# Performance work log

Measured on AMD Instinct MI355X. Metric: run time of the kernel, lower is better.

## Reference

```python
import jax, jax.numpy as jnp
import numpy as np

HID = 128
NUM_HEADS = 8
NUM_LAYERS = 3
N_OP, N_MA, N_JOB = 50000, 1000, 5000
E_SIZES = [150000, 100000, 150000, 100000, 100000]
# (src_type, dst_type) for the 5 edge relations, in module order:
# precedence, assigned_to, can_process, contains, belongs_to
EDGE_SD = [("operation", "operation"), ("operation", "machine"), ("machine", "operation"), ("job", "operation"), ("operation", "job")]
NT_IDX = {"operation": 0, "machine": 1, "job": 2}


def setup_inputs() -> dict:
    key = jax.random.key(0)
    ks = list(jax.random.split(key, 80))
    it = iter(ks)

    def nrm(shape, scale=1.0):
        return jax.random.normal(next(it), shape, dtype=jnp.float32) * scale

    n_nodes = {"operation": N_OP, "machine": N_MA, "job": N_JOB}
    inp = {}
    inp["x_operation"] = nrm((N_OP, 64))
    inp["x_machine"] = nrm((N_MA, 32))
    inp["x_job"] = nrm((N_JOB, 16))
    ei_names = ["ei_prec", "ei_assign", "ei_canproc", "ei_contains", "ei_belongs"]
    ea_names = ["ea_prec", "ea_assign", "ea_canproc", "ea_contains", "ea_belongs"]
    for ne, na, E, (st, dt) in zip(ei_names, ea_names, E_SIZES, EDGE_SD):
        src = jax.random.randint(next(it), (E,), 0, n_nodes[st], dtype=jnp.int32)
        dst = jax.random.randint(next(it), (E,), 0, n_nodes[dt], dtype=jnp.int32)
        inp[ne] = jnp.stack([src, dst])
        inp[na] = nrm((E, 32))
    # node input projections (per-type dims)
    inp["Wn_op"] = nrm((64, HID), 64 ** -0.5)
    inp["bn_op"] = jnp.zeros((HID,), jnp.float32)
    inp["Wn_ma"] = nrm((32, HID), 32 ** -0.5)
    inp["bn_ma"] = jnp.zeros((HID,), jnp.float32)
    inp["Wn_job"] = nrm((16, HID), 16 ** -0.5)
    inp["bn_job"] = jnp.zeros((HID,), jnp.float32)
    # edge attr projections: 5 relations, 32 -> HID, applied once before the layers
    inp["We_proj"] = nrm((5, 32, HID), 32 ** -0.5)
    inp["be_proj"] = jnp.zeros((5, HID), jnp.float32)
    # GATConv params stacked as [layer, edge_type, ...]; heads*out == HID at every layer
    inp["Wg"] = nrm((NUM_LAYERS, 5, HID, HID), HID ** -0.5)      # shared lin for src/dst
    inp["att_s"] = nrm((NUM_LAYERS, 5, HID), HID ** -0.5)
    inp["att_d"] = nrm((NUM_LAYERS, 5, HID), HID ** -0.5)
    inp["Wge"] = nrm((NUM_LAYERS, 5, HID, HID), HID ** -0.5)     # lin_edge
    inp["att_e"] = nrm((NUM_LAYERS, 5, HID), HID ** -0.5)
    inp["bg"] = jnp.zeros((NUM_LAYERS, 5, HID), jnp.float32)      # GATConv output bias
    # BatchNorm affine: [layer, node_type, HID]
    inp["gamma"] = jnp.ones((NUM_LAYERS, 3, HID), jnp.float32)
    inp["beta"] = jnp.zeros((NUM_LAYERS, 3, HID), jnp.float32)
    # output projection for 'operation'
    inp["Wo"] = nrm((HID, HID), HID ** -0.5)
    inp["bo"] = jnp.zeros((HID,), jnp.float32)
    return inp


def _segment_softmax(logits, seg, num):
    # PyG softmax: exp(x - segment_max) / (segment_sum + 1e-16)
    m = jax.ops.segment_max(logits, seg, num_segments=num)
    m = jnp.where(jnp.isfinite(m), m, 0.0)  # empty segments -> 0
    ex = jnp.exp(logits - m[seg])
    den = jax.ops.segment_sum(ex, seg, num_segments=num)
    return ex / (den[seg] + 1e-16)


def _gat_forward(x_operation, x_machine, x_job, eis, eas_raw,
                 Wn_op, bn_op, Wn_ma, bn_ma, Wn_job, bn_job,
                 We_proj, be_proj, Wg, att_s, att_d, Wge, att_e, bg,
                 gamma, beta, Wo, bo):
    x = {
        "operation": x_operation @ Wn_op + bn_op,
        "machine": x_machine @ Wn_ma + bn_ma,
        "job": x_job @ Wn_job + bn_job,
    }
    # edge attrs projected once to HID
    eas = [eas_raw[t] @ We_proj[t] + be_proj[t] for t in range(5)]

    for i in range(NUM_LAYERS):
        H = NUM_HEADS if i < NUM_LAYERS - 1 else 1
        C = HID // H
        resid = x
        agg = {nt: jnp.zeros((x[nt].shape[0], HID), x[nt].dtype) for nt in x}
        for t, (st, dt) in enumerate(EDGE_SD):
            src, dst = eis[t][0], eis[t][1]
            n_dst = x[dt].shape[0]
            xs = (x[st] @ Wg[i, t]).reshape(-1, H, C)            # [Ns,H,C]
            xd = (x[dt] @ Wg[i, t]).reshape(-1, H, C)            # [Nd,H,C]
            a_s = (xs * att_s[i, t].reshape(H, C)).sum(-1)       # [Ns,H]
            a_d = (xd * att_d[i, t].reshape(H, C)).sum(-1)       # [Nd,H]
            e = (eas[t] @ Wge[i, t]).reshape(-1, H, C)           # [E,H,C]
            a_e = (e * att_e[i, t].reshape(H, C)).sum(-1)        # [E,H]
            logits = jax.nn.leaky_relu(a_s[src] + a_d[dst] + a_e, 0.2)
            alpha = _segment_softmax(logits, dst, n_dst)         # [E,H]
            msg = xs[src] * alpha[:, :, None]                    # [E,H,C]
            out = jax.ops.segment_sum(msg, dst, num_segments=n_dst)
            agg[dt] = agg[dt] + out.reshape(n_dst, HID) + bg[i, t]
        new_x = {}
        for nt in x:
            h = agg[nt]
            mu = h.mean(0)
            var = ((h - mu) ** 2).mean(0)  # biased, as BatchNorm1d training
            h = (h - mu) * jax.lax.rsqrt(var + 1e-5) * gamma[i, NT_IDX[nt]] + beta[i, NT_IDX[nt]]
            if i < NUM_LAYERS - 1:
                h = jax.nn.relu(h)  # dropout is identity in eval
            new_x[nt] = h + resid[nt]  # residual (dims always match: HID)
        x = new_x
    return x["operation"] @ Wo + bo


def reference(x_operation, x_machine, x_job,
              ei_prec, ei_assign, ei_canproc, ei_contains, ei_belongs,
              ea_prec, ea_assign, ea_canproc, ea_contains, ea_belongs,
              Wn_op, bn_op, Wn_ma, bn_ma, Wn_job, bn_job,
              We_proj, be_proj, Wg, att_s, att_d, Wge, att_e, bg,
              gamma, beta, Wo, bo):
    eis = [ei_prec, ei_assign, ei_canproc, ei_contains, ei_belongs]
    eas = [ea_prec, ea_assign, ea_canproc, ea_contains, ea_belongs]
    return _gat_forward(x_operation, x_machine, x_job, eis, eas,
                        Wn_op, bn_op, Wn_ma, bn_ma, Wn_job, bn_job,
                        We_proj, be_proj, Wg, att_s, att_d, Wge, att_e, bg,
                        gamma, beta, Wo, bo)
```

## Files before the change

kernel.cpp:

```cpp
#include <hip/hip_runtime.h>
#include <cstdint>

#define HID 128

static constexpr int kNOp = 50000, kNMa = 1000, kNJob = 5000;
static constexpr int kNTot = 56000;
static constexpr int kETot = 600000;
static constexpr int kSeg = 156000;
static constexpr int kEsz[5]   = {150000, 100000, 150000, 100000, 100000};
static constexpr int kSrcT[5]  = {0, 0, 1, 2, 0};
static constexpr int kDstT[5]  = {0, 1, 0, 0, 2};
static constexpr int kNodeOff[3] = {0, 50000, 51000};
static constexpr int kSoff[5]  = {0, 0, 50000, 51000, 0};
static constexpr int kDoff[5]  = {0, 50000, 0, 0, 51000};
static constexpr int kEoff[6]  = {0, 150000, 250000, 400000, 500000, 600000};
static constexpr int kRoff[5]  = {0, 50000, 100000, 101000, 106000};
static constexpr int kRTot = 156000;

typedef __attribute__((ext_vector_type(8))) __bf16 bf16x8;
typedef __attribute__((ext_vector_type(4))) float f32x4;

__device__ inline unsigned short f2b(float f) {
  unsigned u = __float_as_uint(f);
  unsigned r = (u + 0x7FFFu + ((u >> 16) & 1u)) >> 16;
  return (unsigned short)r;
}
__device__ inline float b2f(unsigned short u) {
  return __uint_as_float(((unsigned)u) << 16);
}

__device__ inline int seg_of(int t, int d) {
  if (t == 0) return 3 * d;
  if (t == 2) return 3 * d + 1;
  if (t == 3) return 3 * d + 2;
  if (t == 1) return 150000 + d;
  return 151000 + d;
}

__global__ void conv_pad(const float* __restrict__ in, unsigned short* __restrict__ out,
                         int M, int K, int Kp) {
  int i = blockIdx.x * blockDim.x + threadIdx.x;
  if (i >= M * Kp) return;
  int r = i / Kp, c = i - r * Kp;
  out[i] = (c < K) ? f2b(in[(size_t)r * K + c]) : (unsigned short)0;
}

__global__ void transpose_w(const float* __restrict__ W, unsigned short* __restrict__ Wt,
                            int K, int N, int Kp, int nmat) {
  int i = blockIdx.x * blockDim.x + threadIdx.x;
  int per = N * Kp;
  if (i >= nmat * per) return;
  int b = i / per, rem = i - b * per;
  int n = rem / Kp, k = rem - n * Kp;
  Wt[i] = (k < K) ? f2b(W[(size_t)b * K * N + (size_t)k * N + n]) : (unsigned short)0;
}

template <int KC>
__global__ __launch_bounds__(256) void gemm_mfma(
    const unsigned short* __restrict__ A, const unsigned short* __restrict__ Bt,
    const float* __restrict__ bias, float* __restrict__ Cf,
    unsigned short* __restrict__ Cb, int M) {
  const int K = KC * 32;
  int w = blockIdx.x * 4 + (threadIdx.x >> 6);
  int m0 = w * 16;
  if (m0 >= M) return;
  int lane = threadIdx.x & 63;
  int l16 = lane & 15, quad = lane >> 4;
  int arow = m0 + l16; if (arow >= M) arow = M - 1;
  bf16x8 af[KC];
#pragma unroll
  for (int kc = 0; kc < KC; kc++) {
    int4 raw = *(const int4*)(A + (size_t)arow * K + kc * 32 + quad * 8);
    af[kc] = __builtin_bit_cast(bf16x8, raw);
  }
#pragma unroll
  for (int nt = 0; nt < 8; nt++) {
    int col = nt * 16 + l16;
    f32x4 acc = {0.f, 0.f, 0.f, 0.f};
#pragma unroll
    for (int kc = 0; kc < KC; kc++) {
      int4 braw = *(const int4*)(Bt + (size_t)col * K + kc * 32 + quad * 8);
      acc = __builtin_amdgcn_mfma_f32_16x16x32_bf16(
          af[kc], __builtin_bit_cast(bf16x8, braw), acc, 0, 0, 0);
    }
    float bv = bias ? bias[col] : 0.f;
#pragma unroll
    for (int r = 0; r < 4; r++) {
      int row = m0 + quad * 4 + r;
      if (row < M) {
        float v = acc[r] + bv;
        if (Cf) Cf[(size_t)row * HID + col] = v;
        if (Cb) Cb[(size_t)row * HID + col] = f2b(v);
      }
    }
  }
}

struct GemmJobs {
  const unsigned short* A[5];
  const unsigned short* Bt[5];
  unsigned short* Cb[5];
  int M[5];
  int bpref[6];
};

__global__ __launch_bounds__(256) void gemm_batched(GemmJobs J) {
  int b = blockIdx.x;
  int t = 0;
  while (t < 4 && b >= J.bpref[t + 1]) t++;
  const int M = J.M[t];
  int strip = (b - J.bpref[t]) * 4 + (threadIdx.x >> 6);
  int m0 = strip * 16;
  if (m0 >= M) return;
  int lane = threadIdx.x & 63;
  int l16 = lane & 15, quad = lane >> 4;
  const unsigned short* A = J.A[t];
  const unsigned short* Bt = J.Bt[t];
  unsigned short* Cb = J.Cb[t];
  int arow = m0 + l16; if (arow >= M) arow = M - 1;
  bf16x8 af[4];
#pragma unroll
  for (int kc = 0; kc < 4; kc++) {
    int4 raw = *(const int4*)(A + (size_t)arow * HID + kc * 32 + quad * 8);
    af[kc] = __builtin_bit_cast(bf16x8, raw);
  }
#pragma unroll
  for (int nt = 0; nt < 8; nt++) {
    int col = nt * 16 + l16;
    f32x4 acc = {0.f, 0.f, 0.f, 0.f};
#pragma unroll
    for (int kc = 0; kc < 4; kc++) {
      int4 braw = *(const int4*)(Bt + (size_t)col * HID + kc * 32 + quad * 8);
      acc = __builtin_amdgcn_mfma_f32_16x16x32_bf16(
          af[kc], __builtin_bit_cast(bf16x8, braw), acc, 0, 0, 0);
    }
#pragma unroll
    for (int r = 0; r < 4; r++) {
      int row = m0 + quad * 4 + r;
      if (row < M) Cb[(size_t)row * HID + col] = f2b(acc[r]);
    }
  }
}

template <int NCOL>
__global__ __launch_bounds__(256) void gemm_as(
    const unsigned short* __restrict__ A, const unsigned short* __restrict__ Bt,
    float* __restrict__ out, int M) {
  int w = blockIdx.x * 4 + (threadIdx.x >> 6);
  int m0 = w * 16;
  if (m0 >= M) return;
  int lane = threadIdx.x & 63;
  int l16 = lane & 15, quad = lane >> 4;
  int arow = m0 + l16; if (arow >= M) arow = M - 1;
  bf16x8 af[4];
#pragma unroll
  for (int kc = 0; kc < 4; kc++) {
    int4 raw = *(const int4*)(A + (size_t)arow * HID + kc * 32 + quad * 8);
    af[kc] = __builtin_bit_cast(bf16x8, raw);
  }
#pragma unroll
  for (int nt = 0; nt < NCOL / 16; nt++) {
    int col = nt * 16 + l16;
    f32x4 acc = {0.f, 0.f, 0.f, 0.f};
#pragma unroll
    for (int kc = 0; kc < 4; kc++) {
      int4 braw = *(const int4*)(Bt + (size_t)col * HID + kc * 32 + quad * 8);
      acc = __builtin_amdgcn_mfma_f32_16x16x32_bf16(
          af[kc], __builtin_bit_cast(bf16x8, braw), acc, 0, 0, 0);
    }
#pragma unroll
    for (int r = 0; r < 4; r++) {
      int row = m0 + quad * 4 + r;
      if (row < M) out[(size_t)row * NCOL + col] = acc[r];
    }
  }
}

__global__ void fold_kernel(const float* __restrict__ Wg, const float* __restrict__ att_s,
                            const float* __restrict__ att_d, const float* __restrict__ Wge,
                            const float* __restrict__ att_e, const float* __restrict__ Wep,
                            const float* __restrict__ bep,
                            float* __restrict__ S, float* __restrict__ D,
                            float* __restrict__ w32, float* __restrict__ cvec) {
  int idx = blockIdx.x;
  int h = idx & 7, lt = idx >> 3;
  int l = lt / 5;
  int H = (l < 2) ? 8 : 1, C = HID / H;
  if (h >= H) return;
  int k = threadIdx.x;
  int t = lt % 5;
  const float* wg  = Wg  + (size_t)lt * HID * HID;
  const float* wge = Wge + (size_t)lt * HID * HID;
  const float* as_ = att_s + (size_t)lt * HID + h * C;
  const float* ad_ = att_d + (size_t)lt * HID + h * C;
  const float* ae_ = att_e + (size_t)lt * HID + h * C;
  float s = 0.f, d = 0.f, v = 0.f;
  for (int c = 0; c < C; c++) {
    float wr = wg[(size_t)k * HID + h * C + c];
    s += wr * as_[c];
    d += wr * ad_[c];
    v += wge[(size_t)k * HID + h * C + c] * ae_[c];
  }
  S[(size_t)idx * HID + k] = s;
  D[(size_t)idx * HID + k] = d;
  __shared__ float vs[HID];
  vs[k] = v;
  __syncthreads();
  if (k < 32) {
    const float* wp = Wep + (size_t)t * 32 * HID + (size_t)k * HID;
    float a = 0.f;
    for (int j = 0; j < HID; j++) a += wp[j] * vs[j];
    w32[(size_t)idx * 32 + k] = a;
  }
  if (k == 32) {
    const float* bp = bep + (size_t)t * HID;
    float a = 0.f;
    for (int j = 0; j < HID; j++) a += bp[j] * vs[j];
    cvec[idx] = a;
  }
}

__global__ void build_vb(const float* __restrict__ Sv, const float* __restrict__ Dv,
                         unsigned short* __restrict__ VbT) {
  int i = blockIdx.x * 256 + threadIdx.x;
  if (i >= 3 * 80 * HID) return;
  int l = i / (80 * HID), rem = i % (80 * HID);
  int col = rem / HID, k = rem % HID;
  int H = (l < 2) ? 8 : 1;
  float val = 0.f;
  if (col < 10 * H) {
    int v = col / H, h = col % H;
    const float* base = (v < 5) ? Sv : Dv;
    int t = (v < 5) ? v : v - 5;
    val = base[((size_t)(l * 5 + t) * 8 + h) * HID + k];
  }
  VbT[i] = f2b(val);
}

struct EdgeJobs {
  const int* src[5]; const int* dst[5];
};

__global__ void hist_b(EdgeJobs J, int* __restrict__ cnt) {
  int e = blockIdx.x * 256 + threadIdx.x;
  if (e >= kETot) return;
  int t = 0;
  while (t < 4 && e >= kEoff[t + 1]) t++;
  int d = J.dst[t][e - kEoff[t]];
  atomicAdd(&cnt[seg_of(t, d)], 1);
}

__global__ void scatter_b(EdgeJobs J, int* __restrict__ cursor,
                          int4* __restrict__ edat) {
  int e = blockIdx.x * 256 + threadIdx.x;
  if (e >= kETot) return;
  int t = 0;
  while (t < 4 && e >= kEoff[t + 1]) t++;
  int el = e - kEoff[t];
  int s = J.src[t][el];
  int d = J.dst[t][el];
  int p = atomicAdd(&cursor[seg_of(t, d)], 1);
  edat[p] = make_int4(e, ((s + kSoff[t]) << 3) | t, ((d + kDoff[t]) << 3) | t,
                      s + kRoff[t]);
}

__global__ void scan_blocks(const int* __restrict__ in, int* __restrict__ out,
                            int* __restrict__ bsums, int n) {
  __shared__ int sh[256];
  int t = threadIdx.x;
  int base = blockIdx.x * 1024 + t * 4;
  int v[4]; int s = 0;
#pragma unroll
  for (int j = 0; j < 4; j++) { v[j] = (base + j < n) ? in[base + j] : 0; s += v[j]; }
  sh[t] = s;
  __syncthreads();
  for (int off = 1; off < 256; off <<= 1) {
    int x = (t >= off) ? sh[t - off] : 0;
    __syncthreads();
    sh[t] += x;
    __syncthreads();
  }
  int run = sh[t] - s;
#pragma unroll
  for (int j = 0; j < 4; j++) { if (base + j < n) out[base + j] = run; run += v[j]; }
  if (t == 255) bsums[blockIdx.x] = sh[255];
}

__global__ void scan_carry(int* bsums, int nb, int* sentinel) {
  if (threadIdx.x == 0 && blockIdx.x == 0) {
    int run = 0;
    for (int b = 0; b < nb; b++) { int x = bsums[b]; bsums[b] = run; run += x; }
    *sentinel = run;
  }
}

__global__ void scan_add(int* __restrict__ out, int* __restrict__ cursor,
                         const int* __restrict__ bsums, int n) {
  int base = blockIdx.x * 1024 + threadIdx.x * 4;
  int c = bsums[blockIdx.x];
#pragma unroll
  for (int j = 0; j < 4; j++) {
    if (base + j < n) {
      int v = out[base + j] + c;
      out[base + j] = v;
      cursor[base + j] = v;
    }
  }
}

struct FoldAeJobs {
  const float* ea[5];
  int E[5]; int bpref[6];
};

__global__ __launch_bounds__(256) void fold_ae(FoldAeJobs J, const float* __restrict__ w32,
                                               const float* __restrict__ cv,
                                               float* __restrict__ aet0, float* __restrict__ aet1,
                                               float* __restrict__ aet2) {
  int b = blockIdx.x;
  int t = 0;
  while (t < 4 && b >= J.bpref[t + 1]) t++;
  __shared__ float w[3][8][32];
  __shared__ float cc[3][8];
  for (int i = threadIdx.x; i < 3 * 8 * 32; i += 256) {
    int l = i >> 8, rem = i & 255;
    w[l][rem >> 5][rem & 31] = w32[(size_t)((l * 5 + t) * 8) * 32 + rem];
  }
  if (threadIdx.x < 24) {
    int l = threadIdx.x >> 3, h = threadIdx.x & 7;
    cc[l][h] = cv[(size_t)(l * 5 + t) * 8 + h];
  }
  __syncthreads();
  int e = (b - J.bpref[t]) * 256 + threadIdx.x;
  if (e >= J.E[t]) return;
  int eg = kEoff[t] + e;
  float x[32];
  const float4* p4 = (const float4*)(J.ea[t] + (size_t)e * 32);
#pragma unroll
  for (int i = 0; i < 8; i++) {
    float4 v = p4[i];
    x[4 * i] = v.x; x[4 * i + 1] = v.y; x[4 * i + 2] = v.z; x[4 * i + 3] = v.w;
  }
  float o[8];
#pragma unroll
  for (int h = 0; h < 8; h++) {
    float a = cc[0][h];
#pragma unroll
    for (int k = 0; k < 32; k++) a += x[k] * w[0][h][k];
    o[h] = a;
  }
  float4* d0 = (float4*)(aet0 + (size_t)eg * 8);
  d0[0] = make_float4(o[0], o[1], o[2], o[3]);
  d0[1] = make_float4(o[4], o[5], o[6], o[7]);
#pragma unroll
  for (int h = 0; h < 8; h++) {
    float a = cc[1][h];
#pragma unroll
    for (int k = 0; k < 32; k++) a += x[k] * w[1][h][k];
    o[h] = a;
  }
  float4* d1 = (float4*)(aet1 + (size_t)eg * 8);
  d1[0] = make_float4(o[0], o[1], o[2], o[3]);
  d1[1] = make_float4(o[4], o[5], o[6], o[7]);
  float a = cc[2][0];
#pragma unroll
  for (int k = 0; k < 32; k++) a += x[k] * w[2][0][k];
  aet2[eg] = a;
}

__global__ __launch_bounds__(256) void pass_a8(const int4* __restrict__ edat,
                                               const float* __restrict__ aet,
                                               const float* __restrict__ AS,
                                               float* __restrict__ logits) {
  int p = blockIdx.x * 256 + threadIdx.x;
  if (p >= kETot) return;
  int4 ed = edat[p];
  int e = ed.x, sv = ed.y, dv = ed.z;
  int t = sv & 7;
  const float4* asp = (const float4*)(AS + (size_t)(sv >> 3) * 80 + t * 8);
  const float4* adp = (const float4*)(AS + (size_t)(dv >> 3) * 80 + (5 + t) * 8);
  const float4* aep = (const float4*)(aet + (size_t)e * 8);
  float4 s0 = asp[0], s1 = asp[1];
  float4 d0 = adp[0], d1 = adp[1];
  float4 e0 = aep[0], e1 = aep[1];
  float v[8] = {s0.x + d0.x + e0.x, s0.y + d0.y + e0.y, s0.z + d0.z + e0.z, s0.w + d0.w + e0.w,
                s1.x + d1.x + e1.x, s1.y + d1.y + e1.y, s1.z + d1.z + e1.z, s1.w + d1.w + e1.w};
#pragma unroll
  for (int j = 0; j < 8; j++) v[j] = v[j] > 0.f ? v[j] : 0.2f * v[j];
  float4* L = (float4*)(logits + (size_t)p * 8);
  L[0] = make_float4(v[0], v[1], v[2], v[3]);
  L[1] = make_float4(v[4], v[5], v[6], v[7]);
}

__global__ __launch_bounds__(256) void pass_a1(const int4* __restrict__ edat,
                                               const float* __restrict__ aet2,
                                               const float* __restrict__ AS,
                                               float* __restrict__ logits) {
  int p = blockIdx.x * 256 + threadIdx.x;
  if (p >= kETot) return;
  int4 ed = edat[p];
  int e = ed.x, sv = ed.y, dv = ed.z;
  int t = sv & 7;
  float v = aet2[e] + AS[(size_t)(sv >> 3) * 16 + t] + AS[(size_t)(dv >> 3) * 16 + 5 + t];
  v = v > 0.f ? v : 0.2f * v;
  logits[p] = v;
}

template <int H>
__global__ void softmax_k(const int* __restrict__ rs, float* __restrict__ lg) {
  int g = (int)((blockIdx.x * (size_t)blockDim.x + threadIdx.x) >> 6);
  int lane = threadIdx.x & 63;
  if (g >= kSeg) return;
  int start = rs[g], end = rs[g + 1];
  int n = (end - start) * H;
  if (n == 0) return;
  float* L = lg + (size_t)start * H;
  float m = -3.0e38f;
  for (int idx = lane; idx < n; idx += 64) m = fmaxf(m, L[idx]);
  if (H == 8) {
    m = fmaxf(m, __shfl_xor(m, 8));
    m = fmaxf(m, __shfl_xor(m, 16));
    m = fmaxf(m, __shfl_xor(m, 32));
  } else {
#pragma unroll
    for (int off = 1; off < 64; off <<= 1) m = fmaxf(m, __shfl_xor(m, off));
  }
  float s = 0.f;
  for (int idx = lane; idx < n; idx += 64) {
    float ex = __expf(L[idx] - m);
    L[idx] = ex;
    s += ex;
  }
  if (H == 8) {
    s += __shfl_xor(s, 8);
    s += __shfl_xor(s, 16);
    s += __shfl_xor(s, 32);
  } else {
#pragma unroll
    for (int off = 1; off < 64; off <<= 1) s += __shfl_xor(s, off);
  }
  float inv = 1.f / (s + 1e-16f);
  for (int idx = lane; idx < n; idx += 64) L[idx] *= inv;
}

template <int H>
__global__ void gat_gather_u(const int* __restrict__ rs, const int4* __restrict__ edat,
                             const float* __restrict__ alpha,
                             const unsigned short* __restrict__ xs,
                             float* __restrict__ agg) {
  int g = (int)((blockIdx.x * (size_t)blockDim.x + threadIdx.x) >> 6);
  int lane = threadIdx.x & 63;
  if (g >= kNTot) return;
  int start, end;
  if (g < 50000)      { start = rs[3 * g];              end = rs[3 * g + 3]; }
  else if (g < 51000) { int m = g - 50000; start = rs[150000 + m]; end = rs[150001 + m]; }
  else                { int j = g - 51000; start = rs[151000 + j]; end = rs[151001 + j]; }
  int deg = end - start;
  int l16 = lane & 15, quad = lane >> 4;
  int h = (H == 8) ? (l16 >> 1) : 0;
  float acc[8] = {0.f, 0.f, 0.f, 0.f, 0.f, 0.f, 0.f, 0.f};
  for (int base = 0; base < deg; base += 64) {
    int nchunk = deg - base; if (nchunk > 64) nchunk = 64;
    int sv = (lane < nchunk) ? edat[start + base + lane].w : 0;
    for (int i = 0; i < nchunk; i += 4) {
      int e = i + quad;
      bool act = e < nchunk;
      int s = __shfl(sv, act ? e : 0);
      float w = act ? alpha[(size_t)(start + base + e) * H + h] : 0.f;
      int4 raw = *(const int4*)(xs + (size_t)s * HID + l16 * 8);
      unsigned ua[4] = {(unsigned)raw.x, (unsigned)raw.y, (unsigned)raw.z, (unsigned)raw.w};
#pragma unroll
      for (int j = 0; j < 4; j++) {
        acc[2 * j]     += w * __uint_as_float(ua[j] << 16);
        acc[2 * j + 1] += w * __uint_as_float(ua[j] & 0xFFFF0000u);
      }
    }
  }
#pragma unroll
  for (int j = 0; j < 8; j++) {
    acc[j] += __shfl_xor(acc[j], 16);
    acc[j] += __shfl_xor(acc[j], 32);
  }
  if (quad == 0) {
    float* p = agg + (size_t)g * HID + l16 * 8;
    *(float4*)p = make_float4(acc[0], acc[1], acc[2], acc[3]);
    *(float4*)(p + 4) = make_float4(acc[4], acc[5], acc[6], acc[7]);
  }
}

__global__ void colstats_b(const float* __restrict__ x, float* __restrict__ stats) {
  static constexpr int bpref[4] = {0, 384, 400, 448};
  static constexpr int rowoff[4] = {0, 50000, 51000, 56000};
  int b = blockIdx.x;
  int t = 0;
  while (t < 2 && b >= bpref[t + 1]) t++;
  int bl = b - bpref[t], nb = bpref[t + 1] - bpref[t];
  int tid = threadIdx.x;
  int col = tid & 127, half = tid >> 7;
  float s = 0.f, q = 0.f;
  for (int r = rowoff[t] + bl * 2 + half; r < rowoff[t + 1]; r += nb * 2) {
    float v = x[(size_t)r * HID + col];
    s += v; q += v * v;
  }
  __shared__ float ls[256], lq[256];
  ls[tid] = s; lq[tid] = q;
  __syncthreads();
  if (tid < 128) {
    s = ls[tid] + ls[tid + 128];
    q = lq[tid] + lq[tid + 128];
    unsafeAtomicAdd(&stats[t * 256 + col], s);
    unsafeAtomicAdd(&stats[t * 256 + 128 + col], q);
  }
}

__global__ void bn_apply_b(float* __restrict__ agg, const float* __restrict__ xold,
                           unsigned short* __restrict__ xnb, const float* __restrict__ stats,
                           const float* __restrict__ gammaL, const float* __restrict__ betaL,
                           int relu) {
  size_t i = blockIdx.x * (size_t)blockDim.x + threadIdx.x;
  if (i >= (size_t)kNTot * 32) return;
  int row = (int)(i >> 5);
  int t = (row < 50000) ? 0 : (row < 51000 ? 1 : 2);
  float invN = (t == 0) ? (1.f / 50000.f) : (t == 1 ? (1.f / 1000.f) : (1.f / 5000.f));
  const float* st = stats + t * 256;
  const float* gm = gammaL + t * HID;
  const float* bt = betaL + t * HID;
  int c4 = ((int)(i & 31)) * 4;
  float4 av = ((const float4*)agg)[i];
  float4 xv = ((const float4*)xold)[i];
  float a[4] = {av.x, av.y, av.z, av.w};
  float xo[4] = {xv.x, xv.y, xv.z, xv.w};
  float o[4];
#pragma unroll
  for (int j = 0; j < 4; j++) {
    int c = c4 + j;
    float mu = st[c] * invN;
    float var = st[128 + c] * invN - mu * mu;
    float g = gm[c] * rsqrtf(var + 1e-5f);
    float v = (a[j] - mu) * g + bt[c];
    if (relu) v = fmaxf(v, 0.f);
    o[j] = v + xo[j];
  }
  ((float4*)agg)[i] = make_float4(o[0], o[1], o[2], o[3]);
  ((ushort4*)xnb)[i] = make_ushort4(f2b(o[0]), f2b(o[1]), f2b(o[2]), f2b(o[3]));
}

extern "C" void kernel_launch(void* const* d_in, const int* in_sizes, int n_in,
                              void* d_out, int out_size, void* d_ws, size_t ws_size,
                              hipStream_t stream) {
  const float* x_in[3] = {(const float*)d_in[0], (const float*)d_in[1], (const float*)d_in[2]};
  const int* ei[5];
  const float* ea[5];
  for (int t = 0; t < 5; t++) {
    ei[t] = (const int*)d_in[3 + 2 * t];
    ea[t] = (const float*)d_in[4 + 2 * t];
  }
  const float* Wn[3]  = {(const float*)d_in[13], (const float*)d_in[15], (const float*)d_in[17]};
  const float* bnb[3] = {(const float*)d_in[14], (const float*)d_in[16], (const float*)d_in[18]};
  const float* Wep   = (const float*)d_in[19];
  const float* bep   = (const float*)d_in[20];
  const float* Wg    = (const float*)d_in[21];
  const float* att_s = (const float*)d_in[22];
  const float* att_d = (const float*)d_in[23];
  const float* Wge   = (const float*)d_in[24];
  const float* att_e = (const float*)d_in[25];
  const float* gamma = (const float*)d_in[27];
  const float* beta  = (const float*)d_in[28];
  const float* Wo    = (const float*)d_in[29];
  const float* bo    = (const float*)d_in[30];

  float* ws = (float*)d_ws;
  size_t off = 0;
  auto alloc = [&](size_t n) { size_t o = off; off += (n + 255) & ~(size_t)255; return o; };
  auto allocb = [&](size_t n) { return alloc((n + 1) / 2); };

  float* bufA = ws + alloc((size_t)kNTot * HID);
  float* bufB = ws + alloc((size_t)kNTot * HID);
  unsigned short* xcurb = (unsigned short*)(ws + allocb((size_t)kNTot * HID));
  unsigned short* xs_all = (unsigned short*)(ws + allocb((size_t)kRTot * HID));
  unsigned short* WgT  = (unsigned short*)(ws + allocb((size_t)15 * HID * HID));
  unsigned short* WoT  = (unsigned short*)(ws + allocb((size_t)HID * HID));
  unsigned short* WnT_op  = (unsigned short*)(ws + allocb((size_t)HID * 64));
  unsigned short* WnT_ma  = (unsigned short*)(ws + allocb((size_t)HID * 32));
  unsigned short* WnT_job = (unsigned short*)(ws + allocb((size_t)HID * 32));
  unsigned short* VbT  = (unsigned short*)(ws + allocb((size_t)3 * 80 * HID));
  float* Sv     = ws + alloc((size_t)15 * 8 * HID);
  float* Dv     = ws + alloc((size_t)15 * 8 * HID);
  float* w32    = ws + alloc((size_t)15 * 8 * 32);
  float* cv     = ws + alloc((size_t)15 * 8);
  float* stats  = ws + alloc((size_t)3 * 256);
  float* ASbuf  = ws + alloc((size_t)kNTot * 80);
  float* logits = ws + alloc((size_t)kETot * 8 + 64);
  int* rs_all   = (int*)(ws + alloc((size_t)kSeg + 8));
  int4* edat    = (int4*)(ws + alloc((size_t)kETot * 4));
  float* aet0   = ws + alloc((size_t)kETot * 8);
  float* aet1   = ws + alloc((size_t)kETot * 8);
  float* aet2   = ws + alloc((size_t)kETot);
  unsigned short* xinb_op  = xs_all;
  unsigned short* xinb_ma  = xs_all + 3200000;
  unsigned short* xinb_job = xs_all + 3232000;
  int* cnt    = (int*)logits;
  int* cursor = (int*)(logits + 156032);
  int* bsums  = (int*)(logits + 312064);
  (void)ws_size; (void)in_sizes; (void)n_in; (void)out_size;

  float* xcur = bufA;
  float* agg  = bufB;

  EdgeJobs EJ;
  for (int t = 0; t < 5; t++) { EJ.src[t] = ei[t]; EJ.dst[t] = ei[t] + kEsz[t]; }
  hipMemsetAsync(cnt, 0, (size_t)kSeg * 4, stream);
  hist_b<<<(kETot + 255) / 256, 256, 0, stream>>>(EJ, cnt);
  int nb = (kSeg + 1023) / 1024;
  scan_blocks<<<nb, 256, 0, stream>>>(cnt, rs_all, bsums, kSeg);
  scan_carry<<<1, 64, 0, stream>>>(bsums, nb, rs_all + kSeg);
  scan_add<<<nb, 256, 0, stream>>>(rs_all, cursor, bsums, kSeg);
  scatter_b<<<(kETot + 255) / 256, 256, 0, stream>>>(EJ, cursor, edat);

  conv_pad<<<(kNOp * 64 + 255) / 256, 256, 0, stream>>>(x_in[0], xinb_op, kNOp, 64, 64);
  conv_pad<<<(kNMa * 32 + 255) / 256, 256, 0, stream>>>(x_in[1], xinb_ma, kNMa, 32, 32);
  conv_pad<<<(kNJob * 32 + 255) / 256, 256, 0, stream>>>(x_in[2], xinb_job, kNJob, 16, 32);
  transpose_w<<<(HID * 64 + 255) / 256, 256, 0, stream>>>(Wn[0], WnT_op, 64, HID, 64, 1);
  transpose_w<<<(HID * 32 + 255) / 256, 256, 0, stream>>>(Wn[1], WnT_ma, 32, HID, 32, 1);
  transpose_w<<<(HID * 32 + 255) / 256, 256, 0, stream>>>(Wn[2], WnT_job, 16, HID, 32, 1);
  transpose_w<<<(15 * HID * HID + 255) / 256, 256, 0, stream>>>(Wg, WgT, HID, HID, HID, 15);
  transpose_w<<<(HID * HID + 255) / 256, 256, 0, stream>>>(Wo, WoT, HID, HID, HID, 1);
  fold_kernel<<<120, 128, 0, stream>>>(Wg, att_s, att_d, Wge, att_e, Wep, bep,
                                       Sv, Dv, w32, cv);
  build_vb<<<(3 * 80 * HID + 255) / 256, 256, 0, stream>>>(Sv, Dv, VbT);

  static constexpr int gemmBpref[6]  = {0, 782, 1564, 1580, 1659, 2441};
  static constexpr int foldBpref[6]  = {0, 587, 978, 1565, 1956, 2347};
  static constexpr int nsRel[5] = {50000, 50000, 1000, 5000, 50000};

  FoldAeJobs FJ;
  for (int t = 0; t < 5; t++) {
    FJ.ea[t] = ea[t];
    FJ.E[t] = kEsz[t];
    FJ.bpref[t] = foldBpref[t];
  }
  FJ.bpref[5] = foldBpref[5];
  fold_ae<<<foldBpref[5], 256, 0, stream>>>(FJ, w32, cv, aet0, aet1, aet2);

  gemm_mfma<2><<<((kNOp + 15) / 16 + 3) / 4, 256, 0, stream>>>(
      xinb_op, WnT_op, bnb[0], xcur, xcurb, kNOp);
  gemm_mfma<1><<<((kNMa + 15) / 16 + 3) / 4, 256, 0, stream>>>(
      xinb_ma, WnT_ma, bnb[1], xcur + (size_t)50000 * HID, xcurb + (size_t)50000 * HID, kNMa);
  gemm_mfma<1><<<((kNJob + 15) / 16 + 3) / 4, 256, 0, stream>>>(
      xinb_job, WnT_job, bnb[2], xcur + (size_t)51000 * HID, xcurb + (size_t)51000 * HID, kNJob);

  for (int l = 0; l < 3; l++) {
    int H = (l < 2) ? 8 : 1;

    GemmJobs GJ;
    for (int t = 0; t < 5; t++) {
      int lt = l * 5 + t;
      GJ.A[t]  = xcurb + (size_t)kNodeOff[kSrcT[t]] * HID;
      GJ.Bt[t] = WgT + (size_t)lt * HID * HID;
      GJ.Cb[t] = xs_all + (size_t)kRoff[t] * HID;
      GJ.M[t] = nsRel[t];
      GJ.bpref[t] = gemmBpref[t];
    }
    GJ.bpref[5] = gemmBpref[5];
    gemm_batched<<<gemmBpref[5], 256, 0, stream>>>(GJ);

    int asBlocks = ((kNTot + 15) / 16 + 3) / 4;
    if (H == 8)
      gemm_as<80><<<asBlocks, 256, 0, stream>>>(xcurb, VbT + (size_t)l * 80 * HID, ASbuf, kNTot);
    else
      gemm_as<16><<<asBlocks, 256, 0, stream>>>(xcurb, VbT + (size_t)l * 80 * HID, ASbuf, kNTot);

    int pblocks = (kETot + 255) / 256;
    if (H == 8) {
      const float* aeL = (l == 0) ? aet0 : aet1;
      pass_a8<<<pblocks, 256, 0, stream>>>(edat, aeL, ASbuf, logits);
    } else {
      pass_a1<<<pblocks, 256, 0, stream>>>(edat, aet2, ASbuf, logits);
    }

    if (H == 8) {
      softmax_k<8><<<((size_t)kSeg * 64 + 255) / 256, 256, 0, stream>>>(rs_all, logits);
      gat_gather_u<8><<<((size_t)kNTot * 64 + 255) / 256, 256, 0, stream>>>(
          rs_all, edat, logits, xs_all, agg);
    } else {
      softmax_k<1><<<((size_t)kSeg * 64 + 255) / 256, 256, 0, stream>>>(rs_all, logits);
      gat_gather_u<1><<<((size_t)kNTot * 64 + 255) / 256, 256, 0, stream>>>(
          rs_all, edat, logits, xs_all, agg);
    }

    hipMemsetAsync(stats, 0, 3 * 256 * 4, stream);
    colstats_b<<<448, 256, 0, stream>>>(agg, stats);
    bn_apply_b<<<(unsigned)(((size_t)kNTot * 32 + 255) / 256), 256, 0, stream>>>(
        agg, xcur, xcurb, stats, gamma + (size_t)l * 3 * HID, beta + (size_t)l * 3 * HID,
        (l < 2) ? 1 : 0);
    float* tmp = xcur; xcur = agg; agg = tmp;
  }

  gemm_mfma<4><<<((kNOp + 15) / 16 + 3) / 4, 256, 0, stream>>>(
      xcurb, WoT, bo, (float*)d_out, nullptr, kNOp);
}
```

Baseline: 999.5 us.

## Share operation-row A loads across three relations and vectorize GEMM stores

Replaces the 5-job batched GEMM with a kernel that loads each operation row strip once and computes the three relations whose source is operations (precedence, assigned_to, belongs_to) from the same registers. This cuts the launched blocks from 2441 to 877 and removes redundant A reads. It also swaps the MFMA operand order so each lane holds 4 consecutive output columns of one row, turning scalar stores into vector float4/ushort4 stores in all GEMM kernels. Fewer blocks with three times the work per op-block could lower parallelism and load balance.

```diff
diff --git a/kernel.cpp b/kernel.cpp
--- a/kernel.cpp
+++ b/kernel.cpp
@@ -66,80 +66,80 @@
   if (m0 >= M) return;
   int lane = threadIdx.x & 63;
   int l16 = lane & 15, quad = lane >> 4;
-  int arow = m0 + l16; if (arow >= M) arow = M - 1;
-  bf16x8 af[KC];
+  int xrow = m0 + l16; if (xrow >= M) xrow = M - 1;
+  bf16x8 xf[KC];
 #pragma unroll
   for (int kc = 0; kc < KC; kc++) {
-    int4 raw = *(const int4*)(A + (size_t)arow * K + kc * 32 + quad * 8);
-    af[kc] = __builtin_bit_cast(bf16x8, raw);
-  }
+    int4 raw = *(const int4*)(A + (size_t)xrow * K + kc * 32 + quad * 8);
+    xf[kc] = __builtin_bit_cast(bf16x8, raw);
+  }
+  bool wr = (m0 + l16 < M);
+  int row = m0 + l16;
 #pragma unroll
   for (int nt = 0; nt < 8; nt++) {
-    int col = nt * 16 + l16;
     f32x4 acc = {0.f, 0.f, 0.f, 0.f};
 #pragma unroll
     for (int kc = 0; kc < KC; kc++) {
-      int4 braw = *(const int4*)(Bt + (size_t)col * K + kc * 32 + quad * 8);
+      int4 braw = *(const int4*)(Bt + (size_t)(nt * 16 + l16) * K + kc * 32 + quad * 8);
       acc = __builtin_amdgcn_mfma_f32_16x16x32_bf16(
-          af[kc], __builtin_bit_cast(bf16x8, braw), acc, 0, 0, 0);
-    }
-    float bv = bias ? bias[col] : 0.f;
-#pragma unroll
-    for (int r = 0; r < 4; r++) {
-      int row = m0 + quad * 4 + r;
-      if (row < M) {
-        float v = acc[r] + bv;
-        if (Cf) Cf[(size_t)row * HID + col] = v;
-        if (Cb) Cb[(size_t)row * HID + col] = f2b(v);
-      }
-    }
-  }
-}
-
-struct GemmJobs {
-  const unsigned short* A[5];
-  const unsigned short* Bt[5];
-  unsigned short* Cb[5];
-  int M[5];
-  int bpref[6];
-};
-
-__global__ __launch_bounds__(256) void gemm_batched(GemmJobs J) {
+          __builtin_bit_cast(bf16x8, braw), xf[kc], acc, 0, 0, 0);
+    }
+    int col0 = nt * 16 + quad * 4;
+    float o[4];
+#pragma unroll
+    for (int r = 0; r < 4; r++) o[r] = acc[r] + (bias ? bias[col0 + r] : 0.f);
+    if (wr) {
+      if (Cf) *(float4*)(Cf + (size_t)row * HID + col0) = make_float4(o[0], o[1], o[2], o[3]);
+      if (Cb) *(ushort4*)(Cb + (size_t)row * HID + col0) =
+                  make_ushort4(f2b(o[0]), f2b(o[1]), f2b(o[2]), f2b(o[3]));
+    }
+  }
+}
+
+__global__ __launch_bounds__(256) void gemm_xs(const unsigned short* __restrict__ x,
+                                               const unsigned short* __restrict__ WgTl,
+                                               unsigned short* __restrict__ xs) {
   int b = blockIdx.x;
-  int t = 0;
-  while (t < 4 && b >= J.bpref[t + 1]) t++;
-  const int M = J.M[t];
-  int strip = (b - J.bpref[t]) * 4 + (threadIdx.x >> 6);
+  int grp = (b < 782) ? 0 : (b < 798 ? 1 : 2);
+  int sb   = (grp == 0) ? 0     : (grp == 1 ? 782   : 798);
+  int M    = (grp == 0) ? 50000 : (grp == 1 ? 1000  : 5000);
+  int xoff = (grp == 0) ? 0     : (grp == 1 ? 50000 : 51000);
+  int strip = (b - sb) * 4 + (threadIdx.x >> 6);
   int m0 = strip * 16;
   if (m0 >= M) return;
   int lane = threadIdx.x & 63;
   int l16 = lane & 15, quad = lane >> 4;
-  const unsigned short* A = J.A[t];
-  const unsigned short* Bt = J.Bt[t];
-  unsigned short* Cb = J.Cb[t];
-  int arow = m0 + l16; if (arow >= M) arow = M - 1;
-  bf16x8 af[4];
+  int xrow = m0 + l16; if (xrow >= M) xrow = M - 1;
+  bf16x8 xf[4];
 #pragma unroll
   for (int kc = 0; kc < 4; kc++) {
-    int4 raw = *(const int4*)(A + (size_t)arow * HID + kc * 32 + quad * 8);
-    af[kc] = __builtin_bit_cast(bf16x8, raw);
-  }
-#pragma unroll
-  for (int nt = 0; nt < 8; nt++) {
-    int col = nt * 16 + l16;
-    f32x4 acc = {0.f, 0.f, 0.f, 0.f};
-#pragma unroll
-    for (int kc = 0; kc < 4; kc++) {
-      int4 braw = *(const int4*)(Bt + (size_t)col * HID + kc * 32 + quad * 8);
-      acc = __builtin_amdgcn_mfma_f32_16x16x32_bf16(
-          af[kc], __builtin_bit_cast(bf16x8, braw), acc, 0, 0, 0);
-    }
-#pragma unroll
-    for (int r = 0; r < 4; r++) {
-      int row = m0 + quad * 4 + r;
-      if (row < M) Cb[(size_t)row * HID + col] = f2b(acc[r]);
-    }
-  }
+    int4 raw = *(const int4*)(x + (size_t)(xoff + xrow) * HID + kc * 32 + quad * 8);
+    xf[kc] = __builtin_bit_cast(bf16x8, raw);
+  }
+  bool wr = (m0 + l16 < M);
+  int row = m0 + l16;
+  auto do_rel = [&](int t, int roff) {
+    const unsigned short* Bt = WgTl + (size_t)t * HID * HID;
+    unsigned short* Cb = xs + (size_t)roff * HID;
+#pragma unroll
+    for (int nt = 0; nt < 8; nt++) {
+      f32x4 acc = {0.f, 0.f, 0.f, 0.f};
+#pragma unroll
+      for (int kc = 0; kc < 4; kc++) {
+        int4 braw = *(const int4*)(Bt + (size_t)(nt * 16 + l16) * HID + kc * 32 + quad * 8);
+        acc = __builtin_amdgcn_mfma_f32_16x16x32_bf16(
+            __builtin_bit_cast(bf16x8, braw), xf[kc], acc, 0, 0, 0);
+      }
+      if (wr) {
+        int col0 = nt * 16 + quad * 4;
+        *(ushort4*)(Cb + (size_t)row * HID + col0) =
+            make_ushort4(f2b(acc[0]), f2b(acc[1]), f2b(acc[2]), f2b(acc[3]));
+      }
+    }
+  };
+  if (grp == 0)      { do_rel(0, 0); do_rel(1, 50000); do_rel(4, 106000); }
+  else if (grp == 1) { do_rel(2, 100000); }
+  else               { do_rel(3, 101000); }
 }
 
 template <int NCOL>
@@ -151,27 +151,27 @@
   if (m0 >= M) return;
   int lane = threadIdx.x & 63;
   int l16 = lane & 15, quad = lane >> 4;
-  int arow = m0 + l16; if (arow >= M) arow = M - 1;
-  bf16x8 af[4];
+  int xrow = m0 + l16; if (xrow >= M) xrow = M - 1;
+  bf16x8 xf[4];
 #pragma unroll
   for (int kc = 0; kc < 4; kc++) {
-    int4 raw = *(const int4*)(A + (size_t)arow * HID + kc * 32 + quad * 8);
-    af[kc] = __builtin_bit_cast(bf16x8, raw);
-  }
+    int4 raw = *(const int4*)(A + (size_t)xrow * HID + kc * 32 + quad * 8);
+    xf[kc] = __builtin_bit_cast(bf16x8, raw);
+  }
+  bool wr = (m0 + l16 < M);
+  int row = m0 + l16;
 #pragma unroll
   for (int nt = 0; nt < NCOL / 16; nt++) {
-    int col = nt * 16 + l16;
     f32x4 acc = {0.f, 0.f, 0.f, 0.f};
 #pragma unroll
     for (int kc = 0; kc < 4; kc++) {
-      int4 braw = *(const int4*)(Bt + (size_t)col * HID + kc * 32 + quad * 8);
+      int4 braw = *(const int4*)(Bt + (size_t)(nt * 16 + l16) * HID + kc * 32 + quad * 8);
       acc = __builtin_amdgcn_mfma_f32_16x16x32_bf16(
-          af[kc], __builtin_bit_cast(bf16x8, braw), acc, 0, 0, 0);
-    }
-#pragma unroll
-    for (int r = 0; r < 4; r++) {
-      int row = m0 + quad * 4 + r;
-      if (row < M) out[(size_t)row * NCOL + col] = acc[r];
+          __builtin_bit_cast(bf16x8, braw), xf[kc], acc, 0, 0, 0);
+    }
+    if (wr) {
+      int col0 = nt * 16 + quad * 4;
+      *(float4*)(out + (size_t)row * NCOL + col0) = make_float4(acc[0], acc[1], acc[2], acc[3]);
     }
   }
 }
@@ -629,9 +629,7 @@
                                        Sv, Dv, w32, cv);
   build_vb<<<(3 * 80 * HID + 255) / 256, 256, 0, stream>>>(Sv, Dv, VbT);
 
-  static constexpr int gemmBpref[6]  = {0, 782, 1564, 1580, 1659, 2441};
   static constexpr int foldBpref[6]  = {0, 587, 978, 1565, 1956, 2347};
-  static constexpr int nsRel[5] = {50000, 50000, 1000, 5000, 50000};
 
   FoldAeJobs FJ;
   for (int t = 0; t < 5; t++) {
@@ -652,17 +650,7 @@
   for (int l = 0; l < 3; l++) {
     int H = (l < 2) ? 8 : 1;
 
-    GemmJobs GJ;
-    for (int t = 0; t < 5; t++) {
-      int lt = l * 5 + t;
-      GJ.A[t]  = xcurb + (size_t)kNodeOff[kSrcT[t]] * HID;
-      GJ.Bt[t] = WgT + (size_t)lt * HID * HID;
-      GJ.Cb[t] = xs_all + (size_t)kRoff[t] * HID;
-      GJ.M[t] = nsRel[t];
-      GJ.bpref[t] = gemmBpref[t];
-    }
-    GJ.bpref[5] = gemmBpref[5];
-    gemm_batched<<<gemmBpref[5], 256, 0, stream>>>(GJ);
+    gemm_xs<<<877, 256, 0, stream>>>(xcurb, WgT + (size_t)l * 5 * HID * HID, xs_all);
 
     int asBlocks = ((kNTot + 15) / 16 + 3) / 4;
     if (H == 8)
```

Result: no change. 994.9 us (-0.5%).
